# Kernel optimization log

Hardware: AMD Instinct MI355X
Metric: run time of the kernel (lower is better)

The kernel has to match this reference:

```python
import jax, jax.numpy as jnp
import numpy as np

N, E = 50000, 800000
NODE_DIM, EDGE_DIM = 96, 64
IN_DIM = 2 * NODE_DIM + EDGE_DIM  # 256


def setup_inputs() -> dict:
    key = jax.random.key(0)
    k = jax.random.split(key, 7)
    h = jax.random.normal(k[0], (N, NODE_DIM), dtype=jnp.float32)
    edge_index = jax.random.randint(k[1], (2, E), 0, N, dtype=jnp.int64)
    edge_attr = jax.random.normal(k[2], (E, EDGE_DIM), dtype=jnp.float32)
    # Linear params (PyTorch default-ish scale)
    s = 1.0 / np.sqrt(IN_DIM)
    W_e = jax.random.uniform(k[3], (IN_DIM, NODE_DIM), jnp.float32, -s, s)
    b_e = jax.random.uniform(k[4], (NODE_DIM,), jnp.float32, -s, s)
    W_n = jax.random.uniform(k[5], (IN_DIM, NODE_DIM), jnp.float32, -s, s)
    b_n = jax.random.uniform(k[6], (NODE_DIM,), jnp.float32, -s, s)
    return {"h": h, "edge_index": edge_index, "edge_attr": edge_attr,
            "W_e": W_e, "b_e": b_e, "W_n": W_n, "b_n": b_n}


def reference(h, edge_index, edge_attr, W_e, b_e, W_n, b_n):
    src, dst = edge_index[0], edge_index[1]
    concat = jnp.concatenate([h[src], h[dst], edge_attr], axis=-1)  # [E, 256]
    gates = jax.nn.sigmoid(concat @ W_e + b_e)                      # [E, node_dim]
    messages = jax.nn.softplus(concat @ W_n + b_n)                  # [E, node_dim]
    gated = gates * messages
    n = h.shape[0]
    h_new = jax.ops.segment_sum(gated, dst, num_segments=n)         # [N, node_dim]
    edge_count = jax.ops.segment_sum(jnp.ones((dst.shape[0],), h.dtype), dst, num_segments=n)
    edge_count = jnp.clip(edge_count, 1.0, None)[:, None]
    return h + h_new / edge_count
```

## Files before the change

kernel.cpp:

```cpp
#include <hip/hip_runtime.h>
#include <hip/hip_bf16.h>


#define NODE_DIM 96
#define EDGE_DIM 64
#define IN_DIM   256
#define TILE_E   64
#define NT_TILES 12
#define KT_TILES 8

typedef float  f32x4  __attribute__((ext_vector_type(4)));
typedef __bf16 bf16x8 __attribute__((ext_vector_type(8)));

__device__ __forceinline__ unsigned short bf16rne(float f) {
    unsigned int u = __float_as_uint(f);
    u += 0x7FFFu + ((u >> 16) & 1u);
    return (unsigned short)(u >> 16);
}

__global__ void pack_w_kernel(const float* __restrict__ We,
                              const float* __restrict__ Wn,
                              unsigned short* __restrict__ bpack) {
    int t = blockIdx.x * blockDim.x + threadIdx.x;
    if (t >= KT_TILES * NT_TILES * 64) return;
    int tile = t >> 6, lane = t & 63;
    int kt = tile / NT_TILES, nt = tile % NT_TILES;
    const float* W = (nt < 6) ? We : Wn;
    int n  = (nt % 6) * 16 + (lane & 15);
    int k0 = kt * 32 + (lane >> 4) * 8;
    union { unsigned short u[8]; uint4 v; } tmp;
#pragma unroll
    for (int j = 0; j < 8; ++j) tmp.u[j] = bf16rne(W[(k0 + j) * NODE_DIM + n]);
    *(uint4*)(bpack + (size_t)t * 8) = tmp.v;
}

__global__ __launch_bounds__(256, 4)
void cgconv_main_kernel(const float* __restrict__ h,
                        const int*   __restrict__ eidx,
                        const float* __restrict__ ea,
                        const unsigned short* __restrict__ bpack,
                        const float* __restrict__ be,
                        const float* __restrict__ bn,
                        float* __restrict__ hnew,
                        float* __restrict__ cnt,
                        int E) {
    const int tid  = threadIdx.x;
    const int wave = tid >> 6, lane = tid & 63;
    const int m    = lane & 15;
    const int quad = lane >> 4;

    const int e  = blockIdx.x * TILE_E + wave * 16 + m;
    const int eg = (e < E) ? e : (E - 1);
    const int src = eidx[eg];
    const int dst = eidx[E + eg];

    if (quad == 0 && e < E) unsafeAtomicAdd(cnt + dst, 1.0f);

    f32x4 acc[NT_TILES];
#pragma unroll
    for (int nt = 0; nt < NT_TILES; ++nt) acc[nt] = (f32x4){0.f, 0.f, 0.f, 0.f};

    const float* hsrc = h + (size_t)src * NODE_DIM;
    const float* hdst = h + (size_t)dst * NODE_DIM;
    const float* earo = ea + (size_t)eg * EDGE_DIM;

#pragma unroll
    for (int kt = 0; kt < KT_TILES; ++kt) {
        const int ko = kt * 32 + quad * 8;
        const float* p;
        if (kt < 3)      p = hsrc + ko;
        else if (kt < 6) p = hdst + (ko - NODE_DIM);
        else             p = earo + (ko - 2 * NODE_DIM);
        const float4 v0 = *(const float4*)p;
        const float4 v1 = *(const float4*)(p + 4);
        union { unsigned short u[8]; bf16x8 b; } A;
        A.u[0] = bf16rne(v0.x); A.u[1] = bf16rne(v0.y);
        A.u[2] = bf16rne(v0.z); A.u[3] = bf16rne(v0.w);
        A.u[4] = bf16rne(v1.x); A.u[5] = bf16rne(v1.y);
        A.u[6] = bf16rne(v1.z); A.u[7] = bf16rne(v1.w);
#pragma unroll
        for (int nt = 0; nt < NT_TILES; ++nt) {
            bf16x8 bfrag = *(const bf16x8*)(bpack +
                             (size_t)((kt * NT_TILES + nt) * 64 + lane) * 8);
            acc[nt] = __builtin_amdgcn_mfma_f32_16x16x32_bf16(A.b, bfrag, acc[nt], 0, 0, 0);
        }
    }

    int drow[4], erow[4];
#pragma unroll
    for (int r = 0; r < 4; ++r) {
        drow[r] = __shfl(dst, quad * 4 + r, 64);
        erow[r] = blockIdx.x * TILE_E + wave * 16 + quad * 4 + r;
    }
#pragma unroll
    for (int nt = 0; nt < 6; ++nt) {
        const int col = nt * 16 + m;
        const float bev = be[col];
        const float bnv = bn[col];
#pragma unroll
        for (int r = 0; r < 4; ++r) {
            if (erow[r] >= E) continue;
            float g  = acc[nt][r] + bev;
            float mm = acc[nt + 6][r] + bnv;
            float gate = 1.0f / (1.0f + __expf(-g));
            float sp   = fmaxf(mm, 0.0f) + __logf(1.0f + __expf(-fabsf(mm)));
            unsafeAtomicAdd(hnew + (size_t)drow[r] * NODE_DIM + col, gate * sp);
        }
    }
}

__global__ void finalize_kernel(const float* __restrict__ h,
                                const float* __restrict__ hnew,
                                const float* __restrict__ cnt,
                                float* __restrict__ out,
                                int total4) {
    int i = blockIdx.x * blockDim.x + threadIdx.x;
    if (i >= total4) return;
    int n = i / 24;
    float c = fmaxf(cnt[n], 1.0f);
    float inv = 1.0f / c;
    float4 hv = ((const float4*)h)[i];
    float4 av = ((const float4*)hnew)[i];
    float4 o;
    o.x = hv.x + av.x * inv;
    o.y = hv.y + av.y * inv;
    o.z = hv.z + av.z * inv;
    o.w = hv.w + av.w * inv;
    ((float4*)out)[i] = o;
}

extern "C" void kernel_launch(void* const* d_in, const int* in_sizes, int n_in,
                              void* d_out, int out_size, void* d_ws, size_t ws_size,
                              hipStream_t stream) {
    const float* h   = (const float*)d_in[0];
    const int*   ei  = (const int*)  d_in[1];
    const float* ea  = (const float*)d_in[2];
    const float* We  = (const float*)d_in[3];
    const float* be  = (const float*)d_in[4];
    const float* Wn  = (const float*)d_in[5];
    const float* bn  = (const float*)d_in[6];

    const int N = in_sizes[0] / NODE_DIM;
    const int E = in_sizes[2] / EDGE_DIM;

    char* ws = (char*)d_ws;
    const size_t BPACK_BYTES = (size_t)KT_TILES * NT_TILES * 64 * 8 * 2;
    const size_t CNT_OFF  = BPACK_BYTES;
    const size_t HNEW_OFF = CNT_OFF + (((size_t)N * 4 + 511) / 512) * 512;
    const size_t HNEW_BYTES = (size_t)N * NODE_DIM * 4;

    unsigned short* bpack = (unsigned short*)ws;
    float* cnt  = (float*)(ws + CNT_OFF);
    float* hnew = (float*)(ws + HNEW_OFF);

    hipMemsetAsync(ws + CNT_OFF, 0, HNEW_OFF - CNT_OFF + HNEW_BYTES, stream);

    pack_w_kernel<<<(KT_TILES * NT_TILES * 64 + 255) / 256, 256, 0, stream>>>(We, Wn, bpack);

    const int nblk = (E + TILE_E - 1) / TILE_E;
    cgconv_main_kernel<<<nblk, 256, 0, stream>>>(h, ei, ea, bpack, be, bn, hnew, cnt, E);

    const int total4 = N * (NODE_DIM / 4);
    finalize_kernel<<<(total4 + 255) / 256, 256, 0, stream>>>(h, hnew, cnt, (float*)d_out, total4);
}
```

Baseline: 738.6 us.

## Replace atomic scatter with CSR sort, bf16 message buffer and gather aggregation

Builds a destination-sorted CSR (histogram, three-stage scan, scatter) and splits the main kernel in two. A GEMM kernel computes gated messages for 32 edges per wave and stores them as bf16 per edge. An aggregate kernel then sums each node's incoming messages and writes the output directly. This removes the per-element float atomics into hnew and the separate finalize pass. In exchange it adds several small launches, a large bf16 message buffer that is written and read back, and bf16 rounding of messages. The old atomic path remains as a fallback when the workspace is too small.

```diff
diff --git a/kernel.cpp b/kernel.cpp
--- a/kernel.cpp
+++ b/kernel.cpp
@@ -5,7 +5,6 @@
 #define NODE_DIM 96
 #define EDGE_DIM 64
 #define IN_DIM   256
-#define TILE_E   64
 #define NT_TILES 12
 #define KT_TILES 8
 
@@ -34,26 +33,208 @@
     *(uint4*)(bpack + (size_t)t * 8) = tmp.v;
 }
 
-__global__ __launch_bounds__(256, 4)
-void cgconv_main_kernel(const float* __restrict__ h,
-                        const int*   __restrict__ eidx,
-                        const float* __restrict__ ea,
-                        const unsigned short* __restrict__ bpack,
-                        const float* __restrict__ be,
-                        const float* __restrict__ bn,
-                        float* __restrict__ hnew,
-                        float* __restrict__ cnt,
-                        int E) {
+__global__ void hist_kernel(const int* __restrict__ eidx, unsigned* __restrict__ deg, int E) {
+    int e = blockIdx.x * 256 + threadIdx.x;
+    if (e < E) atomicAdd(deg + eidx[E + e], 1u);
+}
+
+__device__ __forceinline__ unsigned block_excl_scan_256(unsigned v, int tid,
+                                                        unsigned* wsum, unsigned* wpre,
+                                                        unsigned* total) {
+    int lane = tid & 63, w = tid >> 6;
+    unsigned inc = v;
+#pragma unroll
+    for (int o = 1; o < 64; o <<= 1) {
+        unsigned t = __shfl_up(inc, o, 64);
+        if (lane >= o) inc += t;
+    }
+    if (lane == 63) wsum[w] = inc;
+    __syncthreads();
+    if (tid == 0) {
+        unsigned s = 0;
+#pragma unroll
+        for (int k = 0; k < 4; ++k) { wpre[k] = s; s += wsum[k]; }
+        *total = s;
+    }
+    __syncthreads();
+    return inc - v + wpre[w];
+}
+
+__global__ void scan_block_kernel(const unsigned* __restrict__ deg,
+                                  unsigned* __restrict__ scanned,
+                                  unsigned* __restrict__ blocksum, int N) {
+    __shared__ unsigned wsum[4], wpre[4], total;
+    int tid = threadIdx.x;
+    int i = blockIdx.x * 256 + tid;
+    unsigned v = (i < N) ? deg[i] : 0u;
+    unsigned excl = block_excl_scan_256(v, tid, wsum, wpre, &total);
+    if (i < N) scanned[i] = excl;
+    if (tid == 0) blocksum[blockIdx.x] = total;
+}
+
+__global__ void scan_sums_kernel(const unsigned* __restrict__ blocksum,
+                                 unsigned* __restrict__ blockpref, int NB) {
+    __shared__ unsigned wsum[4], wpre[4], total;
+    int tid = threadIdx.x;
+    unsigned v = (tid < NB) ? blocksum[tid] : 0u;
+    unsigned excl = block_excl_scan_256(v, tid, wsum, wpre, &total);
+    if (tid < NB) blockpref[tid] = excl;
+}
+
+__global__ void scan_finalize_kernel(const unsigned* __restrict__ scanned,
+                                     const unsigned* __restrict__ blockpref,
+                                     unsigned* __restrict__ offsets,
+                                     unsigned* __restrict__ cursor, int N, int E) {
+    int i = blockIdx.x * 256 + threadIdx.x;
+    if (i < N) {
+        unsigned o = scanned[i] + blockpref[i >> 8];
+        offsets[i] = o;
+        cursor[i]  = o;
+    }
+    if (i == 0) offsets[N] = (unsigned)E;
+}
+
+__global__ void scatter_kernel(const int* __restrict__ eidx,
+                               unsigned* __restrict__ cursor,
+                               unsigned* __restrict__ sorted, int E) {
+    int e = blockIdx.x * 256 + threadIdx.x;
+    if (e < E) {
+        int d = eidx[E + e];
+        unsigned pos = atomicAdd(cursor + d, 1u);
+        sorted[pos] = (unsigned)e;
+    }
+}
+
+__global__ __launch_bounds__(256)
+void gemm_msg_kernel(const float* __restrict__ h,
+                     const int*   __restrict__ eidx,
+                     const float* __restrict__ ea,
+                     const unsigned short* __restrict__ bpack,
+                     const float* __restrict__ be,
+                     const float* __restrict__ bn,
+                     unsigned short* __restrict__ msg,
+                     int E) {
     const int tid  = threadIdx.x;
     const int wave = tid >> 6, lane = tid & 63;
     const int m    = lane & 15;
     const int quad = lane >> 4;
+    const int base = blockIdx.x * 128 + wave * 32;
+
+    const float* hs[2]; const float* hd[2]; const float* ep[2];
+#pragma unroll
+    for (int mt = 0; mt < 2; ++mt) {
+        int e  = base + mt * 16 + m;
+        int eg = (e < E) ? e : (E - 1);
+        int src = eidx[eg];
+        int dst = eidx[E + eg];
+        hs[mt] = h  + (size_t)src * NODE_DIM;
+        hd[mt] = h  + (size_t)dst * NODE_DIM;
+        ep[mt] = ea + (size_t)eg  * EDGE_DIM;
+    }
+
+    f32x4 acc[2][NT_TILES];
+#pragma unroll
+    for (int mt = 0; mt < 2; ++mt)
+#pragma unroll
+        for (int nt = 0; nt < NT_TILES; ++nt) acc[mt][nt] = (f32x4){0.f, 0.f, 0.f, 0.f};
+
+#pragma unroll
+    for (int kt = 0; kt < KT_TILES; ++kt) {
+        const int ko = kt * 32 + quad * 8;
+        bf16x8 A[2];
+#pragma unroll
+        for (int mt = 0; mt < 2; ++mt) {
+            const float* p;
+            if (kt < 3)      p = hs[mt] + ko;
+            else if (kt < 6) p = hd[mt] + (ko - NODE_DIM);
+            else             p = ep[mt] + (ko - 2 * NODE_DIM);
+            const float4 v0 = *(const float4*)p;
+            const float4 v1 = *(const float4*)(p + 4);
+            union { unsigned short u[8]; bf16x8 b; } t;
+            t.u[0] = bf16rne(v0.x); t.u[1] = bf16rne(v0.y);
+            t.u[2] = bf16rne(v0.z); t.u[3] = bf16rne(v0.w);
+            t.u[4] = bf16rne(v1.x); t.u[5] = bf16rne(v1.y);
+            t.u[6] = bf16rne(v1.z); t.u[7] = bf16rne(v1.w);
+            A[mt] = t.b;
+        }
+#pragma unroll
+        for (int nt = 0; nt < NT_TILES; ++nt) {
+            bf16x8 bfrag = *(const bf16x8*)(bpack +
+                             (size_t)((kt * NT_TILES + nt) * 64 + lane) * 8);
+#pragma unroll
+            for (int mt = 0; mt < 2; ++mt)
+                acc[mt][nt] = __builtin_amdgcn_mfma_f32_16x16x32_bf16(A[mt], bfrag, acc[mt][nt], 0, 0, 0);
+        }
+    }
+
+#pragma unroll
+    for (int nt = 0; nt < 6; ++nt) {
+        const int col = nt * 16 + m;
+        const float bev = be[col];
+        const float bnv = bn[col];
+#pragma unroll
+        for (int mt = 0; mt < 2; ++mt) {
+#pragma unroll
+            for (int r = 0; r < 4; ++r) {
+                const int e = base + mt * 16 + quad * 4 + r;
+                if (e >= E) continue;
+                float g  = acc[mt][nt][r] + bev;
+                float mm = acc[mt][nt + 6][r] + bnv;
+                float gate = 1.0f / (1.0f + __expf(-g));
+                float sp   = fmaxf(mm, 0.0f) + __logf(1.0f + __expf(-fabsf(mm)));
+                msg[(size_t)e * NODE_DIM + col] = bf16rne(gate * sp);
+            }
+        }
+    }
+}
+
+__global__ __launch_bounds__(256)
+void aggregate_kernel(const float* __restrict__ h,
+                      const unsigned* __restrict__ offsets,
+                      const unsigned* __restrict__ sorted,
+                      const unsigned short* __restrict__ msg,
+                      float* __restrict__ out, int N) {
+    const int half = threadIdx.x >> 7;
+    const int col  = threadIdx.x & 127;
+    const int n    = blockIdx.x * 2 + half;
+    if (n >= N || col >= NODE_DIM) return;
+
+    const unsigned o0 = offsets[n];
+    const unsigned o1 = offsets[n + 1];
+    const int deg = (int)(o1 - o0);
+
+    float sum = 0.f;
+    unsigned ecur = (deg > 0) ? sorted[o0] : 0u;
+    for (int k = 0; k < deg; ++k) {
+        unsigned enext = (k + 1 < deg) ? sorted[o0 + k + 1] : ecur;
+        unsigned short u = msg[(size_t)ecur * NODE_DIM + col];
+        sum += __uint_as_float(((unsigned)u) << 16);
+        ecur = enext;
+    }
+    float c = (deg > 0) ? (float)deg : 1.f;
+    out[(size_t)n * NODE_DIM + col] = h[(size_t)n * NODE_DIM + col] + sum / c;
+}
+
+#define TILE_E 64
+__global__ __launch_bounds__(256, 4)
+void cgconv_atomic_kernel(const float* __restrict__ h,
+                          const int*   __restrict__ eidx,
+                          const float* __restrict__ ea,
+                          const unsigned short* __restrict__ bpack,
+                          const float* __restrict__ be,
+                          const float* __restrict__ bn,
+                          float* __restrict__ hnew,
+                          float* __restrict__ cnt,
+                          int E) {
+    const int tid  = threadIdx.x;
+    const int wave = tid >> 6, lane = tid & 63;
+    const int m    = lane & 15;
+    const int quad = lane >> 4;
 
     const int e  = blockIdx.x * TILE_E + wave * 16 + m;
     const int eg = (e < E) ? e : (E - 1);
     const int src = eidx[eg];
     const int dst = eidx[E + eg];
-
     if (quad == 0 && e < E) unsafeAtomicAdd(cnt + dst, 1.0f);
 
     f32x4 acc[NT_TILES];
@@ -117,15 +298,10 @@
     int i = blockIdx.x * blockDim.x + threadIdx.x;
     if (i >= total4) return;
     int n = i / 24;
-    float c = fmaxf(cnt[n], 1.0f);
-    float inv = 1.0f / c;
+    float inv = 1.0f / fmaxf(cnt[n], 1.0f);
     float4 hv = ((const float4*)h)[i];
     float4 av = ((const float4*)hnew)[i];
-    float4 o;
-    o.x = hv.x + av.x * inv;
-    o.y = hv.y + av.y * inv;
-    o.z = hv.z + av.z * inv;
-    o.w = hv.w + av.w * inv;
+    float4 o = {hv.x + av.x * inv, hv.y + av.y * inv, hv.z + av.z * inv, hv.w + av.w * inv};
     ((float4*)out)[i] = o;
 }
 
@@ -142,24 +318,55 @@
 
     const int N = in_sizes[0] / NODE_DIM;
     const int E = in_sizes[2] / EDGE_DIM;
-
     char* ws = (char*)d_ws;
-    const size_t BPACK_BYTES = (size_t)KT_TILES * NT_TILES * 64 * 8 * 2;
-    const size_t CNT_OFF  = BPACK_BYTES;
-    const size_t HNEW_OFF = CNT_OFF + (((size_t)N * 4 + 511) / 512) * 512;
-    const size_t HNEW_BYTES = (size_t)N * NODE_DIM * 4;
-
-    unsigned short* bpack = (unsigned short*)ws;
-    float* cnt  = (float*)(ws + CNT_OFF);
-    float* hnew = (float*)(ws + HNEW_OFF);
-
-    hipMemsetAsync(ws + CNT_OFF, 0, HNEW_OFF - CNT_OFF + HNEW_BYTES, stream);
-
+
+    size_t off = 0;
+    auto take = [&](size_t bytes) { size_t o = off; off = (off + bytes + 511) & ~(size_t)511; return o; };
+    const size_t O_BPACK  = take((size_t)KT_TILES * NT_TILES * 64 * 16);
+    const size_t O_DEG    = take((size_t)N * 4);
+    const size_t O_SCAN   = take((size_t)N * 4);
+    const size_t O_BSUM   = take(1024);
+    const size_t O_BPREF  = take(1024);
+    const size_t O_OFFS   = take((size_t)(N + 1) * 4);
+    const size_t O_CURS   = take((size_t)N * 4);
+    const size_t O_SORTED = take((size_t)E * 4);
+    const size_t O_MSG    = take((size_t)E * NODE_DIM * 2);
+    const size_t NEED = off;
+
+    unsigned short* bpack = (unsigned short*)(ws + O_BPACK);
     pack_w_kernel<<<(KT_TILES * NT_TILES * 64 + 255) / 256, 256, 0, stream>>>(We, Wn, bpack);
 
-    const int nblk = (E + TILE_E - 1) / TILE_E;
-    cgconv_main_kernel<<<nblk, 256, 0, stream>>>(h, ei, ea, bpack, be, bn, hnew, cnt, E);
-
-    const int total4 = N * (NODE_DIM / 4);
-    finalize_kernel<<<(total4 + 255) / 256, 256, 0, stream>>>(h, hnew, cnt, (float*)d_out, total4);
-}
+    if (ws_size >= NEED) {
+        unsigned* deg    = (unsigned*)(ws + O_DEG);
+        unsigned* scn    = (unsigned*)(ws + O_SCAN);
+        unsigned* bsum   = (unsigned*)(ws + O_BSUM);
+        unsigned* bpref  = (unsigned*)(ws + O_BPREF);
+        unsigned* offs   = (unsigned*)(ws + O_OFFS);
+        unsigned* curs   = (unsigned*)(ws + O_CURS);
+        unsigned* sorted = (unsigned*)(ws + O_SORTED);
+        unsigned short* msg = (unsigned short*)(ws + O_MSG);
+
+        hipMemsetAsync(deg, 0, (size_t)N * 4, stream);
+
+        const int NB = (N + 255) / 256;
+        hist_kernel<<<(E + 255) / 256, 256, 0, stream>>>(ei, deg, E);
+        scan_block_kernel<<<NB, 256, 0, stream>>>(deg, scn, bsum, N);
+        scan_sums_kernel<<<1, 256, 0, stream>>>(bsum, bpref, NB);
+        scan_finalize_kernel<<<NB, 256, 0, stream>>>(scn, bpref, offs, curs, N, E);
+        scatter_kernel<<<(E + 255) / 256, 256, 0, stream>>>(ei, curs, sorted, E);
+
+        gemm_msg_kernel<<<(E + 127) / 128, 256, 0, stream>>>(h, ei, ea, bpack, be, bn, msg, E);
+
+        aggregate_kernel<<<(N + 1) / 2, 256, 0, stream>>>(h, offs, sorted, msg, (float*)d_out, N);
+    } else {
+        size_t cnt_off  = O_DEG;
+        size_t hnew_off = (cnt_off + (size_t)N * 4 + 511) & ~(size_t)511;
+        float* cnt  = (float*)(ws + cnt_off);
+        float* hnew = (float*)(ws + hnew_off);
+        hipMemsetAsync(ws + cnt_off, 0, hnew_off - cnt_off + (size_t)N * NODE_DIM * 4, stream);
+        cgconv_atomic_kernel<<<(E + TILE_E - 1) / TILE_E, 256, 0, stream>>>(
+            h, ei, ea, bpack, be, bn, hnew, cnt, E);
+        const int total4 = N * (NODE_DIM / 4);
+        finalize_kernel<<<(total4 + 255) / 256, 256, 0, stream>>>(h, hnew, cnt, (float*)d_out, total4);
+    }
+}
```

Measured after the change: 951.8 us. +28.9%, slower.

## Pre-convert node features to bf16 and process two edge tiles per wave

Applied to the files above, without the earlier changes.

Adds a kernel that converts h to bf16 once, so the per-edge gathers read half as many bytes and skip repeated conversion work. Each wave now handles 32 edges as two M-tiles sharing every B-fragment load, which halves weight-fragment traffic per edge. The epilogue loop is reordered so each destination row's atomics are issued together. The cost is double the accumulator registers (occupancy hint lowered from 4 to 3 blocks per CU) and one extra small kernel launch.

```diff
diff --git a/kernel.cpp b/kernel.cpp
--- a/kernel.cpp
+++ b/kernel.cpp
@@ -5,7 +5,6 @@
 #define NODE_DIM 96
 #define EDGE_DIM 64
 #define IN_DIM   256
-#define TILE_E   64
 #define NT_TILES 12
 #define KT_TILES 8
 
@@ -34,8 +33,22 @@
     *(uint4*)(bpack + (size_t)t * 8) = tmp.v;
 }
 
-__global__ __launch_bounds__(256, 4)
-void cgconv_main_kernel(const float* __restrict__ h,
+__global__ void cvt_h_kernel(const float* __restrict__ h,
+                             unsigned short* __restrict__ hb, int total8) {
+    int i = blockIdx.x * 256 + threadIdx.x;
+    if (i >= total8) return;
+    const float4 v0 = ((const float4*)h)[i * 2];
+    const float4 v1 = ((const float4*)h)[i * 2 + 1];
+    union { unsigned short u[8]; uint4 v; } p;
+    p.u[0] = bf16rne(v0.x); p.u[1] = bf16rne(v0.y);
+    p.u[2] = bf16rne(v0.z); p.u[3] = bf16rne(v0.w);
+    p.u[4] = bf16rne(v1.x); p.u[5] = bf16rne(v1.y);
+    p.u[6] = bf16rne(v1.z); p.u[7] = bf16rne(v1.w);
+    ((uint4*)hb)[i] = p.v;
+}
+
+__global__ __launch_bounds__(256, 3)
+void gemm_atomic_kernel(const unsigned short* __restrict__ hb,
                         const int*   __restrict__ eidx,
                         const float* __restrict__ ea,
                         const unsigned short* __restrict__ bpack,
@@ -48,63 +61,77 @@
     const int wave = tid >> 6, lane = tid & 63;
     const int m    = lane & 15;
     const int quad = lane >> 4;
+    const int base = blockIdx.x * 128 + wave * 32;
 
-    const int e  = blockIdx.x * TILE_E + wave * 16 + m;
-    const int eg = (e < E) ? e : (E - 1);
-    const int src = eidx[eg];
-    const int dst = eidx[E + eg];
+    const unsigned short* hsq[2];
+    const unsigned short* hdq[2];
+    const float*          epq[2];
+    int dstv[2];
+#pragma unroll
+    for (int mt = 0; mt < 2; ++mt) {
+        int e  = base + mt * 16 + m;
+        int eg = (e < E) ? e : (E - 1);
+        int src = eidx[eg];
+        int dst = eidx[E + eg];
+        dstv[mt] = dst;
+        hsq[mt] = hb + (size_t)src * NODE_DIM + quad * 8;
+        hdq[mt] = hb + (size_t)dst * NODE_DIM + quad * 8;
+        epq[mt] = ea + (size_t)eg  * EDGE_DIM + quad * 8;
+        if (quad == 0 && e < E) unsafeAtomicAdd(cnt + dst, 1.0f);
+    }
+    const unsigned short* bl = bpack + lane * 8;
 
-    if (quad == 0 && e < E) unsafeAtomicAdd(cnt + dst, 1.0f);
-
-    f32x4 acc[NT_TILES];
+    f32x4 acc[2][NT_TILES];
 #pragma unroll
-    for (int nt = 0; nt < NT_TILES; ++nt) acc[nt] = (f32x4){0.f, 0.f, 0.f, 0.f};
-
-    const float* hsrc = h + (size_t)src * NODE_DIM;
-    const float* hdst = h + (size_t)dst * NODE_DIM;
-    const float* earo = ea + (size_t)eg * EDGE_DIM;
+    for (int mt = 0; mt < 2; ++mt)
+#pragma unroll
+        for (int nt = 0; nt < NT_TILES; ++nt) acc[mt][nt] = (f32x4){0.f, 0.f, 0.f, 0.f};
 
 #pragma unroll
     for (int kt = 0; kt < KT_TILES; ++kt) {
-        const int ko = kt * 32 + quad * 8;
-        const float* p;
-        if (kt < 3)      p = hsrc + ko;
-        else if (kt < 6) p = hdst + (ko - NODE_DIM);
-        else             p = earo + (ko - 2 * NODE_DIM);
-        const float4 v0 = *(const float4*)p;
-        const float4 v1 = *(const float4*)(p + 4);
-        union { unsigned short u[8]; bf16x8 b; } A;
-        A.u[0] = bf16rne(v0.x); A.u[1] = bf16rne(v0.y);
-        A.u[2] = bf16rne(v0.z); A.u[3] = bf16rne(v0.w);
-        A.u[4] = bf16rne(v1.x); A.u[5] = bf16rne(v1.y);
-        A.u[6] = bf16rne(v1.z); A.u[7] = bf16rne(v1.w);
+        bf16x8 A[2];
+#pragma unroll
+        for (int mt = 0; mt < 2; ++mt) {
+            if (kt < 3) {
+                A[mt] = *(const bf16x8*)(hsq[mt] + kt * 32);
+            } else if (kt < 6) {
+                A[mt] = *(const bf16x8*)(hdq[mt] + (kt - 3) * 32);
+            } else {
+                const float4 v0 = *(const float4*)(epq[mt] + (kt - 6) * 32);
+                const float4 v1 = *(const float4*)(epq[mt] + (kt - 6) * 32 + 4);
+                union { unsigned short u[8]; bf16x8 b; } t;
+                t.u[0] = bf16rne(v0.x); t.u[1] = bf16rne(v0.y);
+                t.u[2] = bf16rne(v0.z); t.u[3] = bf16rne(v0.w);
+                t.u[4] = bf16rne(v1.x); t.u[5] = bf16rne(v1.y);
+                t.u[6] = bf16rne(v1.z); t.u[7] = bf16rne(v1.w);
+                A[mt] = t.b;
+            }
+        }
 #pragma unroll
         for (int nt = 0; nt < NT_TILES; ++nt) {
-            bf16x8 bfrag = *(const bf16x8*)(bpack +
-                             (size_t)((kt * NT_TILES + nt) * 64 + lane) * 8);
-            acc[nt] = __builtin_amdgcn_mfma_f32_16x16x32_bf16(A.b, bfrag, acc[nt], 0, 0, 0);
+            bf16x8 bfrag = *(const bf16x8*)(bl + (kt * NT_TILES + nt) * 512);
+            acc[0][nt] = __builtin_amdgcn_mfma_f32_16x16x32_bf16(A[0], bfrag, acc[0][nt], 0, 0, 0);
+            acc[1][nt] = __builtin_amdgcn_mfma_f32_16x16x32_bf16(A[1], bfrag, acc[1][nt], 0, 0, 0);
         }
     }
 
-    int drow[4], erow[4];
 #pragma unroll
-    for (int r = 0; r < 4; ++r) {
-        drow[r] = __shfl(dst, quad * 4 + r, 64);
-        erow[r] = blockIdx.x * TILE_E + wave * 16 + quad * 4 + r;
-    }
-#pragma unroll
-    for (int nt = 0; nt < 6; ++nt) {
-        const int col = nt * 16 + m;
-        const float bev = be[col];
-        const float bnv = bn[col];
+    for (int mt = 0; mt < 2; ++mt) {
 #pragma unroll
         for (int r = 0; r < 4; ++r) {
-            if (erow[r] >= E) continue;
-            float g  = acc[nt][r] + bev;
-            float mm = acc[nt + 6][r] + bnv;
-            float gate = 1.0f / (1.0f + __expf(-g));
-            float sp   = fmaxf(mm, 0.0f) + __logf(1.0f + __expf(-fabsf(mm)));
-            unsafeAtomicAdd(hnew + (size_t)drow[r] * NODE_DIM + col, gate * sp);
+            const int ee = base + mt * 16 + quad * 4 + r;
+            const int d  = __shfl(dstv[mt], quad * 4 + r, 64);
+            if (ee >= E) continue;
+            float* hrow = hnew + (size_t)d * NODE_DIM;
+#pragma unroll
+            for (int nt = 0; nt < 6; ++nt) {
+                const int col = nt * 16 + m;
+                float g  = acc[mt][nt][r]     + be[col];
+                float mm = acc[mt][nt + 6][r] + bn[col];
+                float gate = 1.0f / (1.0f + __expf(-g));
+                float sp   = fmaxf(mm, 0.0f) + __logf(1.0f + __expf(-fabsf(mm)));
+                unsafeAtomicAdd(hrow + col, gate * sp);
+            }
         }
     }
 }
@@ -117,15 +144,10 @@
     int i = blockIdx.x * blockDim.x + threadIdx.x;
     if (i >= total4) return;
     int n = i / 24;
-    float c = fmaxf(cnt[n], 1.0f);
-    float inv = 1.0f / c;
+    float inv = 1.0f / fmaxf(cnt[n], 1.0f);
     float4 hv = ((const float4*)h)[i];
     float4 av = ((const float4*)hnew)[i];
-    float4 o;
-    o.x = hv.x + av.x * inv;
-    o.y = hv.y + av.y * inv;
-    o.z = hv.z + av.z * inv;
-    o.w = hv.w + av.w * inv;
+    float4 o = {hv.x + av.x * inv, hv.y + av.y * inv, hv.z + av.z * inv, hv.w + av.w * inv};
     ((float4*)out)[i] = o;
 }
 
@@ -142,23 +164,29 @@
 
     const int N = in_sizes[0] / NODE_DIM;
     const int E = in_sizes[2] / EDGE_DIM;
+    char* ws = (char*)d_ws;
 
-    char* ws = (char*)d_ws;
-    const size_t BPACK_BYTES = (size_t)KT_TILES * NT_TILES * 64 * 8 * 2;
-    const size_t CNT_OFF  = BPACK_BYTES;
-    const size_t HNEW_OFF = CNT_OFF + (((size_t)N * 4 + 511) / 512) * 512;
-    const size_t HNEW_BYTES = (size_t)N * NODE_DIM * 4;
+    size_t off = 0;
+    auto take = [&](size_t bytes) { size_t o = off; off = (off + bytes + 511) & ~(size_t)511; return o; };
+    const size_t O_BPACK = take((size_t)KT_TILES * NT_TILES * 64 * 16);
+    const size_t O_CNT   = take((size_t)N * 4);
+    const size_t O_HNEW  = take((size_t)N * NODE_DIM * 4);
+    const size_t O_HB    = take((size_t)N * NODE_DIM * 2);
+    (void)ws_size;
 
-    unsigned short* bpack = (unsigned short*)ws;
-    float* cnt  = (float*)(ws + CNT_OFF);
-    float* hnew = (float*)(ws + HNEW_OFF);
+    unsigned short* bpack = (unsigned short*)(ws + O_BPACK);
+    float* cnt  = (float*)(ws + O_CNT);
+    float* hnew = (float*)(ws + O_HNEW);
+    unsigned short* hb = (unsigned short*)(ws + O_HB);
 
-    hipMemsetAsync(ws + CNT_OFF, 0, HNEW_OFF - CNT_OFF + HNEW_BYTES, stream);
+    hipMemsetAsync(ws + O_CNT, 0, O_HB - O_CNT, stream);
 
     pack_w_kernel<<<(KT_TILES * NT_TILES * 64 + 255) / 256, 256, 0, stream>>>(We, Wn, bpack);
 
-    const int nblk = (E + TILE_E - 1) / TILE_E;
-    cgconv_main_kernel<<<nblk, 256, 0, stream>>>(h, ei, ea, bpack, be, bn, hnew, cnt, E);
+    const int total8 = N * NODE_DIM / 8;
+    cvt_h_kernel<<<(total8 + 255) / 256, 256, 0, stream>>>(h, hb, total8);
+
+    gemm_atomic_kernel<<<(E + 127) / 128, 256, 0, stream>>>(hb, ei, ea, bpack, be, bn, hnew, cnt, E);
 
     const int total4 = N * (NODE_DIM / 4);
     finalize_kernel<<<(total4 + 255) / 256, 256, 0, stream>>>(h, hnew, cnt, (float*)d_out, total4);
```

Result: faster. 698.1 us (-5.5%).
